# Kernel optimization log

Hardware: AMD Instinct MI355X
Metric: run time of the kernel (lower is better)

## Reference

```python
import math
import jax, jax.numpy as jnp
import numpy as np

BATCH, HEAD, LENGTH, D_K = 2, 8, 2048, 128
ROUNDS, N_BUCKETS = 4, 32
NEG_BIG, NEG_SMALL = -1e9, -1e5


def look_back(x):
    # x: [B, n_buckets/2, 2*bl, ...] -> [B, n_buckets/2, 4*bl, ...]
    # shift buckets by one (wrap-around) along bucket axis, concat on chunk axis
    return jnp.concatenate([jnp.roll(x, 1, axis=1), x], axis=2)


def setup_inputs() -> dict:
    key = jax.random.key(0)
    k1, k2, k3 = jax.random.split(key, 3)
    B = BATCH * HEAD
    return {
        "query": jax.random.normal(k1, (BATCH, HEAD, LENGTH, D_K), jnp.float32),
        "value": jax.random.normal(k2, (BATCH, HEAD, LENGTH, D_K), jnp.float32),
        "mask": jnp.ones((BATCH, LENGTH), dtype=bool),
        "rand_matrix": jax.random.normal(k3, (B, D_K, ROUNDS, N_BUCKETS // 2), jnp.float32),
        "seed": 0,
    }


def reference(query, value, mask, rand_matrix, seed):
    batch, head, L, D = query.shape
    B = batch * head
    R = ROUNDS
    nb2 = N_BUCKETS // 2
    bl = L // N_BUCKETS
    bl2, bl4 = 2 * bl, 4 * bl
    bi = jnp.arange(B)[:, None, None]  # batch index for fancy gathers

    # --- LSH hashing ---
    q = query / jnp.linalg.norm(query, axis=-1, keepdims=True)
    fq = q.reshape(B, L, D)
    rm = rand_matrix / jnp.linalg.norm(rand_matrix, axis=1, keepdims=True)
    h = jnp.einsum('bld,bdrk->blrk', fq, rm)          # [B,L,R,nb2]
    hashes = jnp.argmax(jnp.concatenate([h, -h], axis=-1), axis=-1)  # [B,L,R]

    # --- sort tokens by hash (per round) ---
    hash_indices = jnp.argsort(hashes, axis=1)                        # [B,L,R]
    sorted_hashes = jnp.take_along_axis(hashes, hash_indices, axis=1)
    original_indices = jnp.argsort(hash_indices, axis=1)              # inverse perm

    # --- reorder queries into buckets ---
    rq = fq[bi, hash_indices]                  # [B,L,R,D]
    rq = jnp.moveaxis(rq, 2, 3).reshape(B, nb2, bl2, D, R)
    lk = look_back(rq)                         # [B,nb2,bl4,D,R]
    scores = jnp.einsum('bnidr,bnjdr->bnijr', rq, lk) / math.sqrt(D)  # [B,nb2,bl2,bl4,R]

    # --- padding mask ---
    fm = jnp.broadcast_to(mask[:, None, :], (batch, head, L)).reshape(B, L)
    rmask = fm[bi, hash_indices].reshape(B, nb2, bl2, R)
    lb_mask = look_back(rmask)                 # [B,nb2,bl4,R]
    scores = jnp.where(lb_mask[:, :, None, :, :], scores, NEG_BIG)

    # --- same-hash mask ---
    sh = sorted_hashes.reshape(B, nb2, bl2, R)
    lh = look_back(sh)
    scores = jnp.where(sh[:, :, :, None, :] != lh[:, :, None, :, :], NEG_BIG, scores)

    # --- causal + self-attention masks ---
    qi = hash_indices.reshape(B, nb2, bl2, R)
    ki = look_back(qi)                         # [B,nb2,bl4,R]
    scores = jnp.where(qi[:, :, :, None, :] < ki[:, :, None, :, :], NEG_BIG, scores)
    scores = jnp.where(qi[:, :, :, None, :] == ki[:, :, None, :, :], NEG_SMALL, scores)

    # --- duplicate-key counting across rounds ---
    eki = jnp.broadcast_to(ki[:, :, None, :, :], (B, nb2, bl2, bl4, R)).reshape(B, L, bl4, R)
    oi_b = jnp.broadcast_to(original_indices[:, :, None, :], (B, L, bl4, R))
    rki = jnp.take_along_axis(eki, oi_b, axis=1)               # key ids per query, orig order
    flat = rki.reshape(B * L, bl4 * R).astype(jnp.int32)
    order = jnp.argsort(flat, axis=1)
    s = jnp.take_along_axis(flat, order, axis=1)
    counts = jnp.ones(s.shape, jnp.float32)
    for i in range(1, R):
        eq = (s[:, i:] == s[:, :-i]).astype(jnp.float32)
        counts = counts.at[:, i:].add(eq)
        counts = counts.at[:, :-i].add(eq)
    inv = jnp.argsort(order, axis=1)
    count_key = jnp.take_along_axis(counts, inv, axis=1).reshape(B, L, bl4, R)

    # --- softmax over all rounds (dedup-corrected) ---
    scores_flat = scores.reshape(B, L, bl4, R)
    scores_g = jnp.take_along_axis(scores_flat, oi_b, axis=1)
    scores_g = scores_g - jax.lax.stop_gradient(jnp.log(count_key))
    p = jax.nn.softmax(scores_g.reshape(B, L, bl4 * R), axis=-1).reshape(B, L, bl4, R)

    # --- value combine ---
    fv = value.reshape(B, L, D)
    rv = fv[bi, hash_indices]                  # [B,L,R,D]
    rv = jnp.moveaxis(rv, 2, 3).reshape(B, nb2, bl2, D, R)
    lv = look_back(rv)                         # [B,nb2,bl4,D,R]

    ai = jnp.broadcast_to(hash_indices[:, :, None, :], (B, L, bl4, R))
    rp = jnp.take_along_axis(p, ai, axis=1).reshape(B, nb2, bl2, bl4, R)
    att = jnp.einsum('bnijr,bnjdr->bnidr', rp, lv).reshape(B, L, D, R)
    oi_d = jnp.broadcast_to(original_indices[:, :, None, :], (B, L, D, R))
    att = jnp.take_along_axis(att, oi_d, axis=1).sum(axis=-1)  # sum over rounds
    return att.reshape(batch, head, L, D)
```

## Files before the change

kernel.cpp:

```cpp
#include <hip/hip_runtime.h>
#include <hip/hip_bf16.h>
#include <stdint.h>

constexpr int BH  = 16;
constexpr int LEN = 2048;
constexpr int DK  = 128;
constexpr int RND = 4;
constexpr int NB2 = 16;
constexpr int BL2 = 128;

typedef __attribute__((ext_vector_type(8)))  short short8;
typedef __attribute__((ext_vector_type(4)))  float f32x4;
typedef __attribute__((ext_vector_type(16))) float f32x16;

__device__ __forceinline__ float bflo(uint32_t u){ return __uint_as_float(u << 16); }
__device__ __forceinline__ float bfhi(uint32_t u){ return __uint_as_float(u & 0xffff0000u); }
__device__ __forceinline__ uint16_t f2b(float x){
  uint32_t u = __float_as_uint(x);
  return (uint16_t)((u + 0x7fffu + ((u >> 16) & 1u)) >> 16);
}
__device__ __forceinline__ uint32_t pk2(float a, float b){
  return (uint32_t)f2b(a) | ((uint32_t)f2b(b) << 16);
}

__global__ __launch_bounds__(256) void k_hash(const float* __restrict__ q,
    const float* __restrict__ v, const float* __restrict__ rm,
    uint16_t* __restrict__ fqb, uint16_t* __restrict__ vbb,
    uint8_t* __restrict__ hsh)
{
  __shared__ float rm_s[128*64];
  __shared__ float qT[128*64];
  __shared__ float invn_s[64];
  int b = blockIdx.x >> 5, chunk = blockIdx.x & 31;
  int t = threadIdx.x;
  const float4* rm4 = (const float4*)(rm + (size_t)b*8192);
  #pragma unroll
  for (int i=0;i<8;i++) ((float4*)rm_s)[i*256 + t] = rm4[i*256 + t];
  int tl = t >> 2, qq = t & 3;
  int tok = chunk*64 + tl;
  size_t ro = ((size_t)b*LEN + tok)*DK;
  float qs[32];
  float ss = 0.f;
  #pragma unroll
  for (int i=0;i<8;i++){
    float4 w = *(const float4*)(q + ro + qq*32 + i*4);
    qs[i*4]=w.x; qs[i*4+1]=w.y; qs[i*4+2]=w.z; qs[i*4+3]=w.w;
    ss += w.x*w.x + w.y*w.y + w.z*w.z + w.w*w.w;
  }
  ss += __shfl_xor(ss,1); ss += __shfl_xor(ss,2);
  float rn = 1.0f / sqrtf(ss);
  #pragma unroll
  for (int i=0;i<32;i++) qs[i] *= rn;
  #pragma unroll
  for (int i=0;i<4;i++){
    uint4 u;
    u.x = pk2(qs[i*8+0], qs[i*8+1]); u.y = pk2(qs[i*8+2], qs[i*8+3]);
    u.z = pk2(qs[i*8+4], qs[i*8+5]); u.w = pk2(qs[i*8+6], qs[i*8+7]);
    *(uint4*)(fqb + ro + qq*32 + i*8) = u;
  }
  #pragma unroll
  for (int i=0;i<4;i++){
    float4 a = *(const float4*)(v + ro + qq*32 + i*8);
    float4 c = *(const float4*)(v + ro + qq*32 + i*8 + 4);
    uint4 u;
    u.x = pk2(a.x,a.y); u.y = pk2(a.z,a.w); u.z = pk2(c.x,c.y); u.w = pk2(c.z,c.w);
    *(uint4*)(vbb + ro + qq*32 + i*8) = u;
  }
  #pragma unroll
  for (int i=0;i<32;i++) qT[(qq*32+i)*64 + tl] = qs[i];
  __syncthreads();
  if (t < 64){
    float s2 = 0.f;
    for (int d=0; d<128; d++){ float w = rm_s[d*64+t]; s2 += w*w; }
    invn_s[t] = 1.0f / sqrtf(s2);
  }
  int tt = t & 15, cc = t >> 4;
  f32x4 a0={0,0,0,0}, a1={0,0,0,0}, a2={0,0,0,0}, a3={0,0,0,0};
  const float* qTp = qT   + tt*4;
  const float* rmp = rm_s + cc*4;
  #pragma unroll 8
  for (int d=0; d<128; d++){
    float4 qv = *(const float4*)(qTp + d*64);
    float4 rv = *(const float4*)(rmp + d*64);
    a0[0]+=qv.x*rv.x; a0[1]+=qv.x*rv.y; a0[2]+=qv.x*rv.z; a0[3]+=qv.x*rv.w;
    a1[0]+=qv.y*rv.x; a1[1]+=qv.y*rv.y; a1[2]+=qv.y*rv.z; a1[3]+=qv.y*rv.w;
    a2[0]+=qv.z*rv.x; a2[1]+=qv.z*rv.y; a2[2]+=qv.z*rv.z; a2[3]+=qv.z*rv.w;
    a3[0]+=qv.w*rv.x; a3[1]+=qv.w*rv.y; a3[2]+=qv.w*rv.z; a3[3]+=qv.w*rv.w;
  }
  __syncthreads();
  float rin[4];
  #pragma unroll
  for (int j=0;j<4;j++) rin[j] = invn_s[cc*4+j];
  int r = cc >> 2;
  int m = cc & 3;
  float bp[4], bn[4]; int bip[4], bin[4];
  #pragma unroll
  for (int i=0;i<4;i++){ bp[i]=-1e30f; bn[i]=-1e30f; bip[i]=0; bin[i]=16; }
  #pragma unroll
  for (int j=0;j<4;j++){
    int col = m*4 + j;
    #pragma unroll
    for (int i=0;i<4;i++){
      float hv = (i==0?a0[j]:i==1?a1[j]:i==2?a2[j]:a3[j]) * rin[j];
      if ( hv > bp[i]){ bp[i] =  hv; bip[i] = col; }
      if (-hv > bn[i]){ bn[i] = -hv; bin[i] = col + 16; }
    }
  }
  #pragma unroll
  for (int off=16; off<=32; off<<=1){
    #pragma unroll
    for (int i=0;i<4;i++){
      float op = __shfl_xor(bp[i], off); int oip = __shfl_xor(bip[i], off);
      if (op > bp[i] || (op == bp[i] && oip < bip[i])){ bp[i]=op; bip[i]=oip; }
      float on = __shfl_xor(bn[i], off); int oin = __shfl_xor(bin[i], off);
      if (on > bn[i] || (on == bn[i] && oin < bin[i])){ bn[i]=on; bin[i]=oin; }
    }
  }
  if (m == 0){
    uint32_t pk = 0;
    #pragma unroll
    for (int i=0;i<4;i++){
      int bidx = (bn[i] > bp[i]) ? bin[i] : bip[i];
      pk |= (uint32_t)bidx << (8*i);
    }
    *(uint32_t*)(hsh + ((size_t)(b*RND + r))*LEN + chunk*64 + tt*4) = pk;
  }
}

__global__ __launch_bounds__(256) void k_sort(const uint8_t* __restrict__ hsh,
    int* __restrict__ posA, int* __restrict__ tokA)
{
  __shared__ int hist[32*257];
  __shared__ int wtot[4];
  int br = blockIdx.x;
  int t = threadIdx.x;
  const uint8_t* hh = hsh + (size_t)br*LEN;
  uint8_t ub[8];
  #pragma unroll
  for (int i=0;i<8;i++) ub[i] = hh[t*8+i];
  #pragma unroll
  for (int k=0;k<32;k++) hist[k*257+t] = 0;
  __syncthreads();
  #pragma unroll
  for (int i=0;i<8;i++) hist[(int)ub[i]*257 + t] += 1;
  __syncthreads();
  int base = (t>>3)*257 + (t&7)*32, s0 = 0;
  for (int e=0;e<32;e++) s0 += hist[base + ((e + t) & 31)];
  int x = s0;
  #pragma unroll
  for (int off=1; off<64; off<<=1){
    int y = __shfl_up(x, off);
    if ((t & 63) >= off) x += y;
  }
  if ((t & 63) == 63) wtot[t>>6] = x;
  __syncthreads();
  int add = 0;
  #pragma unroll
  for (int i2=0;i2<4;i2++) add += (i2 < (t>>6)) ? wtot[i2] : 0;
  int run = x - s0 + add;
  for (int e=0;e<32;e++){ int tmp = hist[base+e]; hist[base+e] = run; run += tmp; }
  __syncthreads();
  #pragma unroll
  for (int i=0;i<8;i++){
    int l = t*8+i, k = ub[i];
    int p = hist[k*257+t]++;
    posA[(size_t)br*LEN + l] = p;
    tokA[(size_t)br*LEN + p] = l | (k << 11);
  }
}

__global__ __launch_bounds__(256, 3) void k_fattn(
    const uint16_t* __restrict__ fqb, const uint16_t* __restrict__ vbb,
    const int* __restrict__ posA, const int* __restrict__ tokA,
    uint16_t* __restrict__ attb, float* __restrict__ rowsum)
{
  __shared__ __align__(16) char smem[47872];
  uint16_t* Ks0 = (uint16_t*)smem;
  uint16_t* Ks1 = (uint16_t*)(smem + 8704);
  uint16_t* Vs0 = (uint16_t*)(smem + 17408);
  uint16_t* Vs1 = (uint16_t*)(smem + 26112);
  uint16_t* VT  = (uint16_t*)(smem + 34816);
  uint32_t* km4 = (uint32_t*)(smem + 45056);
  uint16_t* tokS= (uint16_t*)(smem + 47104);
  uint16_t* qtokS=(uint16_t*)(smem + 47616);
  uint16_t* Qb  = (uint16_t*)smem;

  int bid0 = blockIdx.x;
  int bid = ((bid0 & 7) << 7) | (bid0 >> 3);
  int n = bid & 15, r = (bid>>4)&3, b = bid>>6;
  int t = threadIdx.x;
  int w = t >> 6, lane = t & 63, l31 = lane & 31, h = lane >> 5;
  int br = b*RND + r;
  int sbase = br*LEN, qs0 = n*BL2;
  size_t gbase = (size_t)b*LEN;

  if (t < 64){
    uint32_t km[4], ck[4], cp[4];
    #pragma unroll
    for (int j=0;j<4;j++){
      int sk4 = t*4 + j;
      int sk = (sk4 < BL2) ? (((n+NB2-1)&15)*BL2 + sk4) : (n*BL2 + sk4 - BL2);
      int raw = tokA[sbase + sk];
      int tok = raw & 2047;
      uint32_t code = 0;
      #pragma unroll
      for (int r2=0;r2<4;r2++){
        int p = posA[(size_t)(b*4+r2)*LEN + tok];
        code |= (uint32_t)(p >> 7) << (4*r2);
      }
      km[j] = (uint32_t)raw & 0xFFFFu;
      ck[j] = code;
      cp[j] = ((code & 0x7777u) + 0x1111u) ^ (code & 0x8888u);
      tokS[sk4] = (uint16_t)tok;
    }
    uint32_t* gp = km4 + t*8;
    gp[0] = km[0] | (km[1]<<16); gp[1] = km[2] | (km[3]<<16);
    gp[2] = ck[0] | (ck[1]<<16); gp[3] = ck[2] | (ck[3]<<16);
    gp[4] = cp[0] | (cp[1]<<16); gp[5] = cp[2] | (cp[3]<<16);
  }
  int raw_q = tokA[sbase + qs0 + w*32 + l31];
  int tokq = raw_q & 2047;
  uint32_t mq16 = (uint32_t)raw_q & 0xFFFFu;
  uint32_t cq = 0;
  #pragma unroll
  for (int r2=0;r2<4;r2++){
    int p = posA[(size_t)(b*4+r2)*LEN + tokq];
    cq |= (uint32_t)(p >> 7) << (4*r2);
  }
  uint32_t mq2 = mq16 | (mq16 << 16);
  uint32_t cq2 = cq | (cq << 16);
  qtokS[w*32 + l31] = (uint16_t)tokq;
  short8 qf[8];
  {
    const uint16_t* qrow = fqb + (gbase + tokq)*DK + h*8;
    #pragma unroll
    for (int dc=0;dc<8;dc++) qf[dc] = *(const short8*)(qrow + dc*16);
  }

  f32x16 O[4];
  #pragma unroll
  for (int i=0;i<4;i++)
    #pragma unroll
    for (int j=0;j<16;j++) O[i][j] = 0.f;
  float rsp = 0.f;

  int srow = t >> 3, sgp = t & 7;
  __syncthreads();
  {
    int tok = (int)tokS[srow];
    const uint16_t* fr = fqb + (gbase + tok)*DK;
    const uint16_t* vr = vbb + (gbase + tok)*DK;
    *(uint4*)(Ks0 + srow*136 + sgp*16)     = *(const uint4*)(fr + sgp*16);
    *(uint4*)(Ks0 + srow*136 + sgp*16 + 8) = *(const uint4*)(fr + sgp*16 + 8);
    *(uint4*)(Vs0 + srow*136 + sgp*16)     = *(const uint4*)(vr + sgp*16);
    *(uint4*)(Vs0 + srow*136 + sgp*16 + 8) = *(const uint4*)(vr + sgp*16 + 8);
  }

  int d2 = t >> 1, kh = t & 1;
  uint16_t* Kc = Ks0; uint16_t* Vc = Vs0;
  uint16_t* Ka = Ks1; uint16_t* Va = Vs1;

  for (int c=0;c<8;c++){
    __syncthreads();
    uint4 kst0, kst1, vst0, vst1;
    if (c < 7){
      int tok = (int)tokS[(c+1)*32 + srow];
      const uint16_t* fr = fqb + (gbase + tok)*DK;
      const uint16_t* vr = vbb + (gbase + tok)*DK;
      kst0 = *(const uint4*)(fr + sgp*16);
      kst1 = *(const uint4*)(fr + sgp*16 + 8);
      vst0 = *(const uint4*)(vr + sgp*16);
      vst1 = *(const uint4*)(vr + sgp*16 + 8);
    }
    f32x16 S;
    #pragma unroll
    for (int j=0;j<16;j++) S[j] = 0.f;
    #pragma unroll
    for (int dc=0;dc<8;dc++){
      short8 a = *(const short8*)(Kc + l31*136 + dc*16 + h*8);
      S = __builtin_amdgcn_mfma_f32_32x32x16_bf16(a, qf[dc], S, 0, 0, 0);
    }
    {
      uint16_t tmp[16];
      #pragma unroll
      for (int jj=0;jj<16;jj++) tmp[jj] = Vc[(kh*16 + jj)*136 + d2];
      *(uint4*)(VT + d2*40 + kh*16)     = *(uint4*)(tmp);
      *(uint4*)(VT + d2*40 + kh*16 + 8) = *(uint4*)(tmp + 8);
    }
    uint32_t u[8];
    #pragma unroll
    for (int g=0; g<4; g++){
      const uint32_t* gp = km4 + (c*8 + 2*g + h)*8;
      uint4 A  = *(const uint4*)gp;
      uint2 Bv = *(const uint2*)(gp + 4);
      #pragma unroll
      for (int p=0; p<2; p++){
        uint32_t kmp = p ? A.y : A.x;
        uint32_t ckp = p ? A.w : A.z;
        uint32_t cpp = p ? Bv.y : Bv.x;
        uint32_t xr2 = mq2 ^ kmp;
        uint32_t x1 = cq2 ^ ckp, x2 = cq2 ^ cpp;
        uint32_t h1 = ~(((x1 & 0x77777777u) + 0x77777777u) | x1) & 0x88888888u;
        uint32_t h2 = ~(((x2 & 0x77777777u) + 0x77777777u) | x2) & 0x88888888u;
        uint32_t prod = ((h1 >> 3) + (h2 >> 3)) * 0x1111u;
        uint32_t xr0 = xr2 & 0xFFFFu, xr1 = xr2 >> 16;
        float rc0 = __builtin_amdgcn_rcpf((float)((prod >> 12) & 15u));
        float rc1 = __builtin_amdgcn_rcpf((float)(prod >> 28));
        float Sv0 = S[g*4 + 2*p], Sv1 = S[g*4 + 2*p + 1];
        float a0 = fmaf(Sv0, 0.12751743f, -0.14426950f);
        float a1 = fmaf(Sv1, 0.12751743f, -0.14426950f);
        a0 = (xr0 == 0u) ? -43.425121f : a0;
        a1 = (xr1 == 0u) ? -43.425121f : a1;
        bool k0 = (xr0 >= 2048u) | (mq16 < (kmp & 0xFFFFu));
        bool k1 = (xr1 >= 2048u) | (mq16 < (kmp >> 16));
        a0 = k0 ? -1e9f : a0;
        a1 = k1 ? -1e9f : a1;
        float e0 = __builtin_amdgcn_exp2f(a0) * rc0;
        float e1 = __builtin_amdgcn_exp2f(a1) * rc1;
        rsp += e0 + e1;
        u[g*2+p] = __builtin_amdgcn_perm(__float_as_uint(e1), __float_as_uint(e0),
                                         0x07060302);
      }
    }
    asm("v_permlane32_swap_b32 %0, %1" : "+v"(u[0]), "+v"(u[2]));
    asm("v_permlane32_swap_b32 %0, %1" : "+v"(u[1]), "+v"(u[3]));
    asm("v_permlane32_swap_b32 %0, %1" : "+v"(u[4]), "+v"(u[6]));
    asm("v_permlane32_swap_b32 %0, %1" : "+v"(u[5]), "+v"(u[7]));
    union { uint32_t wu[4]; short8 v8; } pf0, pf1;
    pf0.wu[0]=u[0]; pf0.wu[1]=u[1]; pf0.wu[2]=u[2]; pf0.wu[3]=u[3];
    pf1.wu[0]=u[4]; pf1.wu[1]=u[5]; pf1.wu[2]=u[6]; pf1.wu[3]=u[7];
    short8 pb0 = pf0.v8, pb1 = pf1.v8;
    __syncthreads();
    if (c < 7){
      *(uint4*)(Ka + srow*136 + sgp*16)     = kst0;
      *(uint4*)(Ka + srow*136 + sgp*16 + 8) = kst1;
      *(uint4*)(Va + srow*136 + sgp*16)     = vst0;
      *(uint4*)(Va + srow*136 + sgp*16 + 8) = vst1;
    }
    #pragma unroll
    for (int dt=0; dt<4; dt++){
      short8 va0 = *(const short8*)(VT + (dt*32 + l31)*40      + h*8);
      short8 va1 = *(const short8*)(VT + (dt*32 + l31)*40 + 16 + h*8);
      O[dt] = __builtin_amdgcn_mfma_f32_32x32x16_bf16(va0, pb0, O[dt], 0, 0, 0);
      O[dt] = __builtin_amdgcn_mfma_f32_32x32x16_bf16(va1, pb1, O[dt], 0, 0, 0);
    }
    uint16_t* tp;
    tp = Kc; Kc = Ka; Ka = tp;
    tp = Vc; Vc = Va; Va = tp;
  }
  rsp += __shfl_xor(rsp, 32);
  if (lane < 32) rowsum[((gbase + tokq) << 2) + r] = rsp;
  #pragma unroll
  for (int p=0;p<2;p++){
    __syncthreads();
    if ((w>>1) == p){
      int qloc = (w&1)*32 + l31;
      #pragma unroll
      for (int dt=0; dt<4; dt++)
        #pragma unroll
        for (int g=0; g<4; g++){
          uint2 ow;
          ow.x = pk2(O[dt][g*4+0], O[dt][g*4+1]);
          ow.y = pk2(O[dt][g*4+2], O[dt][g*4+3]);
          *(uint2*)(Qb + qloc*136 + dt*32 + 8*g + 4*h) = ow;
        }
    }
    __syncthreads();
    #pragma unroll
    for (int i=0;i<4;i++){
      int ch = t + i*256;
      int row = ch >> 4, c16 = ch & 15;
      int otok = (int)qtokS[p*64 + row];
      uint4 u2 = *(const uint4*)(Qb + row*136 + c16*8);
      *(uint4*)(attb + (((gbase + otok) << 2) + r)*DK + c16*8) = u2;
    }
  }
}

__global__ __launch_bounds__(256) void k_out(const uint16_t* __restrict__ attb,
    const float* __restrict__ rowsum, float* __restrict__ out)
{
  int rloc = threadIdx.x >> 5;
  int c4   = (threadIdx.x & 31) * 4;
  int idx  = blockIdx.x*8 + rloc;
  float n0=0.f, n1=0.f, n2=0.f, n3=0.f, den=0.f;
  #pragma unroll
  for (int r=0;r<4;r++){
    size_t ro = ((size_t)idx << 2) + r;
    uint2 u = *(const uint2*)(attb + ro*DK + c4);
    n0 += bflo(u.x); n1 += bfhi(u.x);
    n2 += bflo(u.y); n3 += bfhi(u.y);
    den += rowsum[ro];
  }
  float rd = 1.0f / den;
  float4 o; o.x = n0*rd; o.y = n1*rd; o.z = n2*rd; o.w = n3*rd;
  *(float4*)(out + (size_t)idx*DK + c4) = o;
}

extern "C" void kernel_launch(void* const* d_in, const int* in_sizes, int n_in,
                              void* d_out, int out_size, void* d_ws, size_t ws_size,
                              hipStream_t stream)
{
  const float* q  = (const float*)d_in[0];
  const float* v  = (const float*)d_in[1];
  const float* rm = (const float*)d_in[3];
  float* out = (float*)d_out;

  char* w = (char*)d_ws;
  uint16_t* fqb    = (uint16_t*)(w + 0);
  uint16_t* vbb    = (uint16_t*)(w + 8388608);
  uint8_t*  hsh    = (uint8_t*) (w + 16777216);
  int*      posA   = (int*)     (w + 16908288);
  int*      tokA   = (int*)     (w + 17432576);
  float*    rowsum = (float*)   (w + 18481152);
  uint16_t* attb   = (uint16_t*)(w + 19005440);

  k_hash <<<dim3(BH*32),      dim3(256), 0, stream>>>(q, v, rm, fqb, vbb, hsh);
  k_sort <<<dim3(BH*RND),     dim3(256), 0, stream>>>(hsh, posA, tokA);
  k_fattn<<<dim3(BH*RND*NB2), dim3(256), 0, stream>>>(fqb, vbb, posA, tokA, attb, rowsum);
  k_out  <<<dim3(BH*LEN/8),   dim3(256), 0, stream>>>(attb, rowsum, out);
}
```

Baseline: 157.6 us.

## Store V transposed and swizzled directly into double-buffered LDS, drop per-chunk transpose

V rows fetched from global memory are now scattered straight into a transposed, XOR-swizzled LDS layout with double buffering, instead of being staged row-major and then transposed through LDS each chunk. This removes one LDS round-trip and one __syncthreads per chunk, and shrinks shared memory, which may allow higher occupancy. In exchange, the writes become 16 scalar 16-bit LDS stores per thread, which could cause bank conflicts or extra instruction overhead.

```diff
diff --git a/kernel.cpp b/kernel.cpp
--- a/kernel.cpp
+++ b/kernel.cpp
@@ -174,15 +174,14 @@
     const int* __restrict__ posA, const int* __restrict__ tokA,
     uint16_t* __restrict__ attb, float* __restrict__ rowsum)
 {
-  __shared__ __align__(16) char smem[47872];
+  __shared__ __align__(16) char smem[40704];
   uint16_t* Ks0 = (uint16_t*)smem;
   uint16_t* Ks1 = (uint16_t*)(smem + 8704);
-  uint16_t* Vs0 = (uint16_t*)(smem + 17408);
-  uint16_t* Vs1 = (uint16_t*)(smem + 26112);
-  uint16_t* VT  = (uint16_t*)(smem + 34816);
-  uint32_t* km4 = (uint32_t*)(smem + 45056);
-  uint16_t* tokS= (uint16_t*)(smem + 47104);
-  uint16_t* qtokS=(uint16_t*)(smem + 47616);
+  uint16_t* VT0 = (uint16_t*)(smem + 17408);
+  uint16_t* VT1 = (uint16_t*)(smem + 27648);
+  uint32_t* km4 = (uint32_t*)(smem + 37888);
+  uint16_t* tokS= (uint16_t*)(smem + 39936);
+  uint16_t* qtokS=(uint16_t*)(smem + 40448);
   uint16_t* Qb  = (uint16_t*)smem;
 
   int bid0 = blockIdx.x;
@@ -245,6 +244,7 @@
   float rsp = 0.f;
 
   int srow = t >> 3, sgp = t & 7;
+  int swz_kv = (srow & 7) + 8*((srow >> 3) ^ (sgp & 3));
   __syncthreads();
   {
     int tok = (int)tokS[srow];
@@ -252,13 +252,19 @@
     const uint16_t* vr = vbb + (gbase + tok)*DK;
     *(uint4*)(Ks0 + srow*136 + sgp*16)     = *(const uint4*)(fr + sgp*16);
     *(uint4*)(Ks0 + srow*136 + sgp*16 + 8) = *(const uint4*)(fr + sgp*16 + 8);
-    *(uint4*)(Vs0 + srow*136 + sgp*16)     = *(const uint4*)(vr + sgp*16);
-    *(uint4*)(Vs0 + srow*136 + sgp*16 + 8) = *(const uint4*)(vr + sgp*16 + 8);
-  }
-
-  int d2 = t >> 1, kh = t & 1;
-  uint16_t* Kc = Ks0; uint16_t* Vc = Vs0;
-  uint16_t* Ka = Ks1; uint16_t* Va = Vs1;
+    uint4 v0 = *(const uint4*)(vr + sgp*16);
+    uint4 v1 = *(const uint4*)(vr + sgp*16 + 8);
+    uint16_t* vt = VT0 + (sgp*16)*40 + swz_kv;
+    uint32_t vv[8] = {v0.x,v0.y,v0.z,v0.w,v1.x,v1.y,v1.z,v1.w};
+    #pragma unroll
+    for (int i2=0;i2<8;i2++){
+      vt[(2*i2)*40]   = (uint16_t)(vv[i2] & 0xFFFFu);
+      vt[(2*i2+1)*40] = (uint16_t)(vv[i2] >> 16);
+    }
+  }
+
+  uint16_t* Kc = Ks0; uint16_t* Vc = VT0;
+  uint16_t* Ka = Ks1; uint16_t* Va = VT1;
 
   for (int c=0;c<8;c++){
     __syncthreads();
@@ -279,13 +285,6 @@
     for (int dc=0;dc<8;dc++){
       short8 a = *(const short8*)(Kc + l31*136 + dc*16 + h*8);
       S = __builtin_amdgcn_mfma_f32_32x32x16_bf16(a, qf[dc], S, 0, 0, 0);
-    }
-    {
-      uint16_t tmp[16];
-      #pragma unroll
-      for (int jj=0;jj<16;jj++) tmp[jj] = Vc[(kh*16 + jj)*136 + d2];
-      *(uint4*)(VT + d2*40 + kh*16)     = *(uint4*)(tmp);
-      *(uint4*)(VT + d2*40 + kh*16 + 8) = *(uint4*)(tmp + 8);
     }
     uint32_t u[8];
     #pragma unroll
@@ -330,19 +329,25 @@
     pf0.wu[0]=u[0]; pf0.wu[1]=u[1]; pf0.wu[2]=u[2]; pf0.wu[3]=u[3];
     pf1.wu[0]=u[4]; pf1.wu[1]=u[5]; pf1.wu[2]=u[6]; pf1.wu[3]=u[7];
     short8 pb0 = pf0.v8, pb1 = pf1.v8;
-    __syncthreads();
+    #pragma unroll
+    for (int dt=0; dt<4; dt++){
+      int dd = dt*32 + l31;
+      int dx = (dd >> 4) & 3;
+      short8 va0 = *(const short8*)(Vc + dd*40 + 8*(h ^ dx));
+      short8 va1 = *(const short8*)(Vc + dd*40 + 8*((2 + h) ^ dx));
+      O[dt] = __builtin_amdgcn_mfma_f32_32x32x16_bf16(va0, pb0, O[dt], 0, 0, 0);
+      O[dt] = __builtin_amdgcn_mfma_f32_32x32x16_bf16(va1, pb1, O[dt], 0, 0, 0);
+    }
     if (c < 7){
       *(uint4*)(Ka + srow*136 + sgp*16)     = kst0;
       *(uint4*)(Ka + srow*136 + sgp*16 + 8) = kst1;
-      *(uint4*)(Va + srow*136 + sgp*16)     = vst0;
-      *(uint4*)(Va + srow*136 + sgp*16 + 8) = vst1;
-    }
-    #pragma unroll
-    for (int dt=0; dt<4; dt++){
-      short8 va0 = *(const short8*)(VT + (dt*32 + l31)*40      + h*8);
-      short8 va1 = *(const short8*)(VT + (dt*32 + l31)*40 + 16 + h*8);
-      O[dt] = __builtin_amdgcn_mfma_f32_32x32x16_bf16(va0, pb0, O[dt], 0, 0, 0);
-      O[dt] = __builtin_amdgcn_mfma_f32_32x32x16_bf16(va1, pb1, O[dt], 0, 0, 0);
+      uint16_t* vt = Va + (sgp*16)*40 + swz_kv;
+      uint32_t vv[8] = {vst0.x,vst0.y,vst0.z,vst0.w,vst1.x,vst1.y,vst1.z,vst1.w};
+      #pragma unroll
+      for (int i2=0;i2<8;i2++){
+        vt[(2*i2)*40]   = (uint16_t)(vv[i2] & 0xFFFFu);
+        vt[(2*i2+1)*40] = (uint16_t)(vv[i2] >> 16);
+      }
     }
     uint16_t* tp;
     tp = Kc; Kc = Ka; Ka = tp;
```

After: 154.9 us. No clear change (-1.7%).
